# Optimization experiments

Measured on AMD Instinct MI355X. Metric: run time of the kernel, lower is better.

The kernel has to match this reference:

```python
import jax, jax.numpy as jnp
from jax import lax
import numpy as np

P = 24  # skip distance

def setup_inputs() -> dict:
    key = jax.random.key(0)
    k1, k2, k3 = jax.random.split(key, 3)
    B, T, F, U = 256, 192, 512, 512
    x = jax.random.normal(k1, (B, T, F), dtype=jnp.float32)
    # Glorot-ish scaled params (scale keeps relu candidate from exploding)
    kernel = jax.random.normal(k2, (F, 3 * U), dtype=jnp.float32) * (1.0 / np.sqrt(F))
    recurrent_kernel = jax.random.normal(k3, (U, 3 * U), dtype=jnp.float32) * (1.0 / np.sqrt(U))
    input_bias = jnp.zeros((3 * U,), dtype=jnp.float32)
    recurrent_bias = jnp.zeros((3 * U,), dtype=jnp.float32)
    return {"x": x, "kernel": kernel, "recurrent_kernel": recurrent_kernel,
            "input_bias": input_bias, "recurrent_bias": recurrent_bias}

def _gru_step(h, xc, kernel, recurrent_kernel, input_bias, recurrent_bias):
    # h, xc: [B, p, U] / [B, p, F] -- p independent skip-chains run as extra batch
    mx = xc @ kernel + input_bias            # [B, p, 3U]
    mi = h @ recurrent_kernel + recurrent_bias  # [B, p, 3U] (reset_after=True)
    xz, xr, xh = jnp.split(mx, 3, axis=-1)
    rz, rr, rh = jnp.split(mi, 3, axis=-1)
    z = jax.nn.sigmoid(xz + rz)
    r = jax.nn.sigmoid(xr + rr)
    hh = jax.nn.relu(xh + r * rh)            # activation='relu'
    return z * h + (1.0 - z) * hh

def reference(x, kernel, recurrent_kernel, input_bias, recurrent_bias):
    B, T, F = x.shape
    U = kernel.shape[1] // 3
    nc = T // P  # T chosen as multiple of p
    # chunk c, lane j  <->  timestep c*p + j; predecessor of (c, j) is (c-1, j) = t - p
    xs = x.reshape(B, nc, P, F).transpose(1, 0, 2, 3)  # [nc, B, p, F]
    h0 = jnp.zeros((B, P, U), dtype=x.dtype)

    def step(h, xc):
        hn = _gru_step(h, xc, kernel, recurrent_kernel, input_bias, recurrent_bias)
        return hn, hn

    _, ys = lax.scan(step, h0, xs)                      # [nc, B, p, U]
    outputs = ys.transpose(1, 0, 2, 3).reshape(B, T, U)  # [B, T, U]
    # return_sequences=False, return_state=False -> last timestep output
    return outputs[:, -1, :]
```

## Files before the change

### kernel.cpp

```cpp
#include <hip/hip_runtime.h>
#include <hip/hip_bf16.h>
#include <math.h>


typedef float f32x4 __attribute__((ext_vector_type(4)));
typedef short short8 __attribute__((ext_vector_type(8)));

#define BB 256
#define UU 512
#define KK 512
#define N3 1536

__device__ __forceinline__ float sigmoidf_(float s) {
    return 1.0f / (1.0f + __expf(-s));
}

__global__ __launch_bounds__(256)
void prologue(const float* __restrict__ ker, const float* __restrict__ rker,
              const float* __restrict__ x,
              __hip_bfloat16* __restrict__ Kt, __hip_bfloat16* __restrict__ Rtb,
              __hip_bfloat16* __restrict__ Xb)
{
    __shared__ float tile[32][33];
    const int blk = blockIdx.x;
    const int tid = threadIdx.x;
    if (blk < 1536) {
        const float* W = (blk < 768) ? ker : rker;
        __hip_bfloat16* Wt = (blk < 768) ? Kt : Rtb;
        const int b = (blk < 768) ? blk : blk - 768;
        const int xx = tid & 31, yy = tid >> 5;
        const int c0 = (b % 48) * 32;
        const int r0 = (b / 48) * 32;
        #pragma unroll
        for (int i = 0; i < 32; i += 8)
            tile[yy + i][xx] = W[(long)(r0 + yy + i) * N3 + c0 + xx];
        __syncthreads();
        #pragma unroll
        for (int i = 0; i < 32; i += 8)
            Wt[(long)(c0 + yy + i) * KK + r0 + xx] = __float2bfloat16(tile[xx][yy + i]);
    } else {
        const int idx = (blk - 1536) * 256 + tid;
        const int e = idx * 8;
        const int m = e >> 9;
        const int kk = e & 511;
        const int bb = m & 255, c = m >> 8;
        const float* src = x + (long)bb * (192 * 512) + (long)(c * 24 + 23) * 512 + kk;
        float4 v0 = *(const float4*)src;
        float4 v1 = *(const float4*)(src + 4);
        __hip_bfloat16* dst = Xb + (long)m * 512 + kk;
        dst[0] = __float2bfloat16(v0.x);
        dst[1] = __float2bfloat16(v0.y);
        dst[2] = __float2bfloat16(v0.z);
        dst[3] = __float2bfloat16(v0.w);
        dst[4] = __float2bfloat16(v1.x);
        dst[5] = __float2bfloat16(v1.y);
        dst[6] = __float2bfloat16(v1.z);
        dst[7] = __float2bfloat16(v1.w);
    }
}

__global__ __launch_bounds__(256)
void gemm_mx(const __hip_bfloat16* __restrict__ A,
             const __hip_bfloat16* __restrict__ Bt,
             const float* __restrict__ bias,
             float* __restrict__ C)
{
    __shared__ char Als[4096];
    __shared__ char Bls[8192];
    const int tid = threadIdx.x;
    const int lane = tid & 63;
    const int w = tid >> 6;
    const int wm = w >> 1, wn = w & 1;
    const int m0 = blockIdx.y * 64;
    const int n0 = blockIdx.x * 128;
    const int lr = lane & 15;
    const int hi = lane >> 4;

    const int srow = lane >> 2;
    const int scol = (lane & 3) * 16;

    const char* Ab = (const char*)A;
    const char* Bb = (const char*)Bt;

    f32x4 acc[2][4];
    #pragma unroll
    for (int i = 0; i < 2; ++i)
        #pragma unroll
        for (int j = 0; j < 4; ++j) acc[i][j] = {0.f, 0.f, 0.f, 0.f};

    for (int ks = 0; ks < 16; ++ks) {
        const long k0b = (long)ks * 64;
        __syncthreads();
        __builtin_amdgcn_global_load_lds(
            (const __attribute__((address_space(1))) unsigned int*)
                (Ab + (long)(m0 + w * 16 + srow) * 1024 + k0b + scol),
            (__attribute__((address_space(3))) unsigned int*)(Als + w * 1024),
            16, 0, 0);
        #pragma unroll
        for (int j = 0; j < 2; ++j)
            __builtin_amdgcn_global_load_lds(
                (const __attribute__((address_space(1))) unsigned int*)
                    (Bb + (long)(n0 + w * 32 + j * 16 + srow) * 1024 + k0b + scol),
                (__attribute__((address_space(3))) unsigned int*)
                    (Bls + (w * 2 + j) * 1024),
                16, 0, 0);
        __syncthreads();

        short8 a[2], b[4];
        #pragma unroll
        for (int i = 0; i < 2; ++i)
            a[i] = *(const short8*)(Als + (wm * 32 + i * 16 + lr) * 64 + hi * 16);
        #pragma unroll
        for (int j = 0; j < 4; ++j)
            b[j] = *(const short8*)(Bls + (wn * 64 + j * 16 + lr) * 64 + hi * 16);
        #pragma unroll
        for (int i = 0; i < 2; ++i)
            #pragma unroll
            for (int j = 0; j < 4; ++j)
                acc[i][j] = __builtin_amdgcn_mfma_f32_16x16x32_bf16(
                    a[i], b[j], acc[i][j], 0, 0, 0);
    }

    #pragma unroll
    for (int i = 0; i < 2; ++i)
        #pragma unroll
        for (int j = 0; j < 4; ++j) {
            const int u = n0 + wn * 64 + j * 16 + lr;
            const float bi = bias[u];
            #pragma unroll
            for (int q = 0; q < 4; ++q)
                C[(long)(m0 + wm * 32 + i * 16 + hi * 4 + q) * N3 + u]
                    = acc[i][j][q] + bi;
        }
}

__global__ __launch_bounds__(256)
void gru_step(const __hip_bfloat16* __restrict__ Rt,
              const float* __restrict__ rbias,
              const float* __restrict__ MXc,
              const char* __restrict__ hb_in,
              const float* __restrict__ hf_in,
              char* __restrict__ hb_out,
              float* __restrict__ hf_out,
              float* __restrict__ out,
              int last)
{
    __shared__ char Bls[96 * 1024];
    __shared__ char Als[32 * 1024];
    __shared__ char MXls[12288];
    const int tid = threadIdx.x;
    const int lane = tid & 63;
    const int w = tid >> 6;
    const int wy = w >> 1, wx = w & 1;
    const int by = blockIdx.x & 7;
    const int bx = blockIdx.x >> 3;
    const int lr = lane & 15;
    const int hi = lane >> 4;
    const int m0 = by * 32 + wy * 16;
    const int n0 = bx * 32;
    const int u  = n0 + wx * 16 + lr;

    {
        const char* RtB = (const char*)Rt;
        #pragma unroll
        for (int i = 0; i < 24; ++i) {
            const int j  = i * 4 + w;
            const int gt = j >> 5, cc = j & 31;
            const long srcoff = (long)(gt * 512 + n0 + cc) * 1024
                              + ((lane * 16) ^ ((j & 7) << 4));
            __builtin_amdgcn_global_load_lds(
                (const __attribute__((address_space(1))) unsigned int*)(RtB + srcoff),
                (__attribute__((address_space(3))) unsigned int*)(Bls + (long)j * 1024),
                16, 0, 0);
        }
    }
    #pragma unroll
    for (int i = 0; i < 8; ++i) {
        const int j = i * 4 + w;
        __builtin_amdgcn_global_load_lds(
            (const __attribute__((address_space(1))) unsigned int*)
                (hb_in + (long)(by * 32 + j) * 1024 + lane * 16),
            (__attribute__((address_space(3))) unsigned int*)(Als + (long)j * 1024),
            16, 0, 0);
    }
    {
        const char* MXb = (const char*)MXc;
        #pragma unroll
        for (int jj = 0; jj < 3; ++jj) {
            const int k = w + 4 * jj;
            const int gt = k >> 2, rblk = k & 3;
            const long src = (long)(by * 32 + rblk * 8 + (lane >> 3)) * 6144
                           + gt * 2048 + bx * 128 + (lane & 7) * 16;
            __builtin_amdgcn_global_load_lds(
                (const __attribute__((address_space(1))) unsigned int*)(MXb + src),
                (__attribute__((address_space(3))) unsigned int*)
                    (MXls + gt * 4096 + rblk * 1024),
                16, 0, 0);
        }
    }

    float hold[4];
    #pragma unroll
    for (int q = 0; q < 4; ++q)
        hold[q] = hf_in[(long)(m0 + hi * 4 + q) * UU + u];
    const float rbz = rbias[u];
    const float rbg = rbias[u + UU];
    const float rbh = rbias[u + 2 * UU];

    __syncthreads();

    f32x4 acc[3] = {{0.f,0.f,0.f,0.f},{0.f,0.f,0.f,0.f},{0.f,0.f,0.f,0.f}};
    #pragma unroll
    for (int kk = 0; kk < 16; ++kk) {
        const short8 a = *(const short8*)(Als + (wy * 16 + lr) * 1024
            + ((kk * 64 + hi * 16) ^ ((lr & 7) << 4)));
        #pragma unroll
        for (int gt = 0; gt < 3; ++gt) {
            const short8 b = *(const short8*)(Bls
                + (long)(gt * 32 + wx * 16 + lr) * 1024
                + ((kk * 64 + hi * 16) ^ ((lr & 7) << 4)));
            acc[gt] = __builtin_amdgcn_mfma_f32_16x16x32_bf16(a, b, acc[gt], 0, 0, 0);
        }
    }

    #pragma unroll
    for (int q = 0; q < 4; ++q) {
        const int rloc = wy * 16 + hi * 4 + q;
        const float xz = *(const float*)(MXls + 0 * 4096 + rloc * 128 + (wx * 16 + lr) * 4);
        const float xr = *(const float*)(MXls + 1 * 4096 + rloc * 128 + (wx * 16 + lr) * 4);
        const float xh = *(const float*)(MXls + 2 * 4096 + rloc * 128 + (wx * 16 + lr) * 4);
        const float z = sigmoidf_(xz + acc[0][q] + rbz);
        const float r = sigmoidf_(xr + acc[1][q] + rbg);
        const float cand = xh + r * (acc[2][q] + rbh);
        const float hh = fmaxf(cand, 0.0f);
        const float hn = z * hold[q] + (1.0f - z) * hh;
        const int m = m0 + hi * 4 + q;
        if (!last) {
            union { __hip_bfloat16 bf; unsigned short s; } cv;
            cv.bf = __float2bfloat16(hn);
            *(unsigned short*)(hb_out + (long)m * 1024
                + ((u * 2) ^ ((m & 7) << 4))) = cv.s;
            hf_out[(long)m * UU + u] = hn;
        } else {
            out[(long)m * UU + u] = hn;
        }
    }
}

__global__ __launch_bounds__(256)
void gru_step1(const __hip_bfloat16* __restrict__ Rt,
               const float* __restrict__ rbias,
               const float* __restrict__ MX1,
               const float* __restrict__ MX0,
               char* __restrict__ hb_out,
               float* __restrict__ hf_out)
{
    __shared__ char Bls[96 * 1024];
    __shared__ char Als[32 * 1024];
    __shared__ char MXls[12288];
    __shared__ float patchls[32 * 32];
    const int tid = threadIdx.x;
    const int lane = tid & 63;
    const int w = tid >> 6;
    const int wy = w >> 1, wx = w & 1;
    const int by = blockIdx.x & 7;
    const int bx = blockIdx.x >> 3;
    const int lr = lane & 15;
    const int hi = lane >> 4;
    const int m0 = by * 32 + wy * 16;
    const int n0 = bx * 32;
    const int u  = n0 + wx * 16 + lr;

    {
        const char* RtB = (const char*)Rt;
        #pragma unroll
        for (int i = 0; i < 24; ++i) {
            const int j  = i * 4 + w;
            const int gt = j >> 5, cc = j & 31;
            const long srcoff = (long)(gt * 512 + n0 + cc) * 1024
                              + ((lane * 16) ^ ((j & 7) << 4));
            __builtin_amdgcn_global_load_lds(
                (const __attribute__((address_space(1))) unsigned int*)(RtB + srcoff),
                (__attribute__((address_space(3))) unsigned int*)(Bls + (long)j * 1024),
                16, 0, 0);
        }
    }
    {
        const char* MXb = (const char*)MX1;
        #pragma unroll
        for (int jj = 0; jj < 3; ++jj) {
            const int k = w + 4 * jj;
            const int gt = k >> 2, rblk = k & 3;
            const long src = (long)(by * 32 + rblk * 8 + (lane >> 3)) * 6144
                           + gt * 2048 + bx * 128 + (lane & 7) * 16;
            __builtin_amdgcn_global_load_lds(
                (const __attribute__((address_space(1))) unsigned int*)(MXb + src),
                (__attribute__((address_space(3))) unsigned int*)
                    (MXls + gt * 4096 + rblk * 1024),
                16, 0, 0);
        }
    }
    const float rbz = rbias[u];
    const float rbg = rbias[u + UU];
    const float rbh = rbias[u + 2 * UU];

    {
        const int rt = tid >> 3;
        const int cb = (tid & 7) * 64;
        const float* mrow = MX0 + (long)(by * 32 + rt) * N3;
        #pragma unroll 4
        for (int j = 0; j < 64; j += 4) {
            const int col = cb + j;
            float4 xz = *(const float4*)(mrow + col);
            float4 xr = *(const float4*)(mrow + UU + col);
            float4 xh = *(const float4*)(mrow + 2 * UU + col);
            float4 bz = *(const float4*)(rbias + col);
            float4 br = *(const float4*)(rbias + UU + col);
            float4 bh = *(const float4*)(rbias + 2 * UU + col);
            float hv[4];
            hv[0] = (1.0f - sigmoidf_(xz.x + bz.x)) * fmaxf(xh.x + sigmoidf_(xr.x + br.x) * bh.x, 0.0f);
            hv[1] = (1.0f - sigmoidf_(xz.y + bz.y)) * fmaxf(xh.y + sigmoidf_(xr.y + br.y) * bh.y, 0.0f);
            hv[2] = (1.0f - sigmoidf_(xz.z + bz.z)) * fmaxf(xh.z + sigmoidf_(xr.z + br.z) * bh.z, 0.0f);
            hv[3] = (1.0f - sigmoidf_(xz.w + bz.w)) * fmaxf(xh.w + sigmoidf_(xr.w + br.w) * bh.w, 0.0f);
            #pragma unroll
            for (int e = 0; e < 4; ++e) {
                const int cc = col + e;
                union { __hip_bfloat16 bf; unsigned short s; } cv;
                cv.bf = __float2bfloat16(hv[e]);
                *(unsigned short*)(Als + rt * 1024 + ((cc * 2) ^ ((rt & 7) << 4))) = cv.s;
                if (cc >= n0 && cc < n0 + 32)
                    patchls[rt * 32 + (cc - n0)] = hv[e];
            }
        }
    }

    __syncthreads();

    f32x4 acc[3] = {{0.f,0.f,0.f,0.f},{0.f,0.f,0.f,0.f},{0.f,0.f,0.f,0.f}};
    #pragma unroll
    for (int kk = 0; kk < 16; ++kk) {
        const short8 a = *(const short8*)(Als + (wy * 16 + lr) * 1024
            + ((kk * 64 + hi * 16) ^ ((lr & 7) << 4)));
        #pragma unroll
        for (int gt = 0; gt < 3; ++gt) {
            const short8 b = *(const short8*)(Bls
                + (long)(gt * 32 + wx * 16 + lr) * 1024
                + ((kk * 64 + hi * 16) ^ ((lr & 7) << 4)));
            acc[gt] = __builtin_amdgcn_mfma_f32_16x16x32_bf16(a, b, acc[gt], 0, 0, 0);
        }
    }

    #pragma unroll
    for (int q = 0; q < 4; ++q) {
        const int rloc = wy * 16 + hi * 4 + q;
        const float xz = *(const float*)(MXls + 0 * 4096 + rloc * 128 + (wx * 16 + lr) * 4);
        const float xr = *(const float*)(MXls + 1 * 4096 + rloc * 128 + (wx * 16 + lr) * 4);
        const float xh = *(const float*)(MXls + 2 * 4096 + rloc * 128 + (wx * 16 + lr) * 4);
        const float hv = patchls[rloc * 32 + wx * 16 + lr];
        const float z = sigmoidf_(xz + acc[0][q] + rbz);
        const float r = sigmoidf_(xr + acc[1][q] + rbg);
        const float cand = xh + r * (acc[2][q] + rbh);
        const float hh = fmaxf(cand, 0.0f);
        const float hn = z * hv + (1.0f - z) * hh;
        const int m = m0 + hi * 4 + q;
        union { __hip_bfloat16 bf; unsigned short s; } cv;
        cv.bf = __float2bfloat16(hn);
        *(unsigned short*)(hb_out + (long)m * 1024
            + ((u * 2) ^ ((m & 7) << 4))) = cv.s;
        hf_out[(long)m * UU + u] = hn;
    }
}

extern "C" void kernel_launch(void* const* d_in, const int* in_sizes, int n_in,
                              void* d_out, int out_size, void* d_ws, size_t ws_size,
                              hipStream_t stream)
{
    const float* x     = (const float*)d_in[0];
    const float* ker   = (const float*)d_in[1];
    const float* rker  = (const float*)d_in[2];
    const float* ibias = (const float*)d_in[3];
    const float* rbias = (const float*)d_in[4];
    float* out = (float*)d_out;

    char* ws = (char*)d_ws;
    float*          MX   = (float*)ws;
    __hip_bfloat16* Xb   = (__hip_bfloat16*)(ws + 12582912);
    __hip_bfloat16* Kt   = (__hip_bfloat16*)(ws + 14680064);
    __hip_bfloat16* Rt   = (__hip_bfloat16*)(ws + 16252928);
    char*           hb0  = (char*)(ws + 17825792);
    char*           hb1  = (char*)(ws + 18087936);
    float*          hf0  = (float*)(ws + 12582912);
    float*          hf1  = (float*)(ws + 13107200);

    prologue<<<2048, 256, 0, stream>>>(ker, rker, x, Kt, Rt, Xb);

    gemm_mx<<<dim3(N3 / 128, 2048 / 64), 256, 0, stream>>>(Xb, Kt, ibias, MX);

    gru_step1<<<128, 256, 0, stream>>>(Rt, rbias, MX + (long)BB * N3, MX,
                                       hb0, hf0);

    for (int c = 2; c < 8; ++c) {
        const char*  hb_in = (c & 1) ? hb1 : hb0;
        const float* hf_in = (c & 1) ? hf1 : hf0;
        char*  hb_o = (c & 1) ? hb0 : hb1;
        float* hf_o = (c & 1) ? hf0 : hf1;
        gru_step<<<128, 256, 0, stream>>>(
            Rt, rbias, MX + (long)c * BB * N3, hb_in, hf_in,
            hb_o, hf_o, out, (c == 7) ? 1 : 0);
    }
}
```

Before: 66.97 us.

## Overlap input-projection GEMM tiles with recurrent GRU steps in shared launches

Splits the big input-projection GEMM so only the first two chunks are computed up front. The remaining chunks are computed by extra blocks appended to each recurrent step launch, one chunk ahead. Step 0 becomes a simple elementwise kernel, since h is zero, that also carries GEMM tiles, which removes the fused step-1 special case. The aim is to fill the idle CUs during the small 128-block recurrent steps and cut the serial GEMM time. In exchange, the GEMM blocks share the large LDS footprint of the step kernel, and the hf buffers move to a new workspace region.

```diff
diff --git a/kernel.cpp b/kernel.cpp
--- a/kernel.cpp
+++ b/kernel.cpp
@@ -59,23 +59,17 @@
     }
 }
 
-__global__ __launch_bounds__(256)
-void gemm_mx(const __hip_bfloat16* __restrict__ A,
-             const __hip_bfloat16* __restrict__ Bt,
-             const float* __restrict__ bias,
-             float* __restrict__ C)
-{
-    __shared__ char Als[4096];
-    __shared__ char Bls[8192];
+__device__ __forceinline__ void gemm_tile_dev(
+    const __hip_bfloat16* __restrict__ A, const __hip_bfloat16* __restrict__ Bt,
+    const float* __restrict__ bias, float* __restrict__ C,
+    int m0, int n0, char* Als, char* Bls)
+{
     const int tid = threadIdx.x;
     const int lane = tid & 63;
     const int w = tid >> 6;
     const int wm = w >> 1, wn = w & 1;
-    const int m0 = blockIdx.y * 64;
-    const int n0 = blockIdx.x * 128;
     const int lr = lane & 15;
     const int hi = lane >> 4;
-
     const int srow = lane >> 2;
     const int scol = (lane & 3) * 16;
 
@@ -132,6 +126,168 @@
                 C[(long)(m0 + wm * 32 + i * 16 + hi * 4 + q) * N3 + u]
                     = acc[i][j][q] + bi;
         }
+}
+
+__global__ __launch_bounds__(256)
+void gemm_mx(const __hip_bfloat16* __restrict__ A,
+             const __hip_bfloat16* __restrict__ Bt,
+             const float* __restrict__ bias,
+             float* __restrict__ C)
+{
+    __shared__ char Als[4096];
+    __shared__ char Bls[8192];
+    gemm_tile_dev(A, Bt, bias, C, blockIdx.y * 64, blockIdx.x * 128, Als, Bls);
+}
+
+__global__ __launch_bounds__(256)
+void gru_step0g(const float* __restrict__ MX0,
+                const float* __restrict__ rbias,
+                float* __restrict__ hf_out,
+                char* __restrict__ hb_out,
+                const __hip_bfloat16* __restrict__ Xb,
+                const __hip_bfloat16* __restrict__ Kt,
+                const float* __restrict__ ibias,
+                float* __restrict__ MX)
+{
+    __shared__ char GA[4096];
+    __shared__ char GB[8192];
+    if (blockIdx.x >= 512) {
+        const int g = blockIdx.x - 512;
+        const int gx = g % 12, gy = g / 12;
+        gemm_tile_dev(Xb, Kt, ibias, MX, 2 * 256 + gy * 64, gx * 128, GA, GB);
+        return;
+    }
+    const int idx = blockIdx.x * 256 + threadIdx.x;
+    const int b = idx >> 9;
+    const int u = idx & 511;
+    const float* mx = MX0 + (long)b * N3;
+    const float z = sigmoidf_(mx[u]          + rbias[u]);
+    const float r = sigmoidf_(mx[u + UU]     + rbias[u + UU]);
+    const float cand = mx[u + 2 * UU] + r * rbias[u + 2 * UU];
+    const float hh = fmaxf(cand, 0.0f);
+    const float hn = (1.0f - z) * hh;
+    hf_out[idx] = hn;
+    union { __hip_bfloat16 bf; unsigned short s; } cv;
+    cv.bf = __float2bfloat16(hn);
+    *(unsigned short*)(hb_out + (long)b * 1024 + ((u * 2) ^ ((b & 7) << 4))) = cv.s;
+}
+
+__global__ __launch_bounds__(256)
+void gru_stepg(const __hip_bfloat16* __restrict__ Rt,
+               const float* __restrict__ rbias,
+               const float* __restrict__ MXc,
+               const char* __restrict__ hb_in,
+               const float* __restrict__ hf_in,
+               char* __restrict__ hb_out,
+               float* __restrict__ hf_out,
+               const __hip_bfloat16* __restrict__ Xb,
+               const __hip_bfloat16* __restrict__ Kt,
+               const float* __restrict__ ibias,
+               float* __restrict__ MX,
+               int cg)
+{
+    __shared__ char Bls[96 * 1024];
+    __shared__ char Als[32 * 1024];
+    __shared__ char MXls[12288];
+    if (blockIdx.x >= 128) {
+        const int g = blockIdx.x - 128;
+        const int gx = g % 12, gy = g / 12;
+        gemm_tile_dev(Xb, Kt, ibias, MX, cg * 256 + gy * 64, gx * 128, Als, Bls);
+        return;
+    }
+    const int tid = threadIdx.x;
+    const int lane = tid & 63;
+    const int w = tid >> 6;
+    const int wy = w >> 1, wx = w & 1;
+    const int by = blockIdx.x & 7;
+    const int bx = blockIdx.x >> 3;
+    const int lr = lane & 15;
+    const int hi = lane >> 4;
+    const int m0 = by * 32 + wy * 16;
+    const int n0 = bx * 32;
+    const int u  = n0 + wx * 16 + lr;
+
+    {
+        const char* RtB = (const char*)Rt;
+        #pragma unroll
+        for (int i = 0; i < 24; ++i) {
+            const int j  = i * 4 + w;
+            const int gt = j >> 5, cc = j & 31;
+            const long srcoff = (long)(gt * 512 + n0 + cc) * 1024
+                              + ((lane * 16) ^ ((j & 7) << 4));
+            __builtin_amdgcn_global_load_lds(
+                (const __attribute__((address_space(1))) unsigned int*)(RtB + srcoff),
+                (__attribute__((address_space(3))) unsigned int*)(Bls + (long)j * 1024),
+                16, 0, 0);
+        }
+    }
+    #pragma unroll
+    for (int i = 0; i < 8; ++i) {
+        const int j = i * 4 + w;
+        __builtin_amdgcn_global_load_lds(
+            (const __attribute__((address_space(1))) unsigned int*)
+                (hb_in + (long)(by * 32 + j) * 1024 + lane * 16),
+            (__attribute__((address_space(3))) unsigned int*)(Als + (long)j * 1024),
+            16, 0, 0);
+    }
+    {
+        const char* MXb = (const char*)MXc;
+        #pragma unroll
+        for (int jj = 0; jj < 3; ++jj) {
+            const int k = w + 4 * jj;
+            const int gt = k >> 2, rblk = k & 3;
+            const long src = (long)(by * 32 + rblk * 8 + (lane >> 3)) * 6144
+                           + gt * 2048 + bx * 128 + (lane & 7) * 16;
+            __builtin_amdgcn_global_load_lds(
+                (const __attribute__((address_space(1))) unsigned int*)(MXb + src),
+                (__attribute__((address_space(3))) unsigned int*)
+                    (MXls + gt * 4096 + rblk * 1024),
+                16, 0, 0);
+        }
+    }
+
+    float hold[4];
+    #pragma unroll
+    for (int q = 0; q < 4; ++q)
+        hold[q] = hf_in[(long)(m0 + hi * 4 + q) * UU + u];
+    const float rbz = rbias[u];
+    const float rbg = rbias[u + UU];
+    const float rbh = rbias[u + 2 * UU];
+
+    __syncthreads();
+
+    f32x4 acc[3] = {{0.f,0.f,0.f,0.f},{0.f,0.f,0.f,0.f},{0.f,0.f,0.f,0.f}};
+    #pragma unroll
+    for (int kk = 0; kk < 16; ++kk) {
+        const short8 a = *(const short8*)(Als + (wy * 16 + lr) * 1024
+            + ((kk * 64 + hi * 16) ^ ((lr & 7) << 4)));
+        #pragma unroll
+        for (int gt = 0; gt < 3; ++gt) {
+            const short8 b = *(const short8*)(Bls
+                + (long)(gt * 32 + wx * 16 + lr) * 1024
+                + ((kk * 64 + hi * 16) ^ ((lr & 7) << 4)));
+            acc[gt] = __builtin_amdgcn_mfma_f32_16x16x32_bf16(a, b, acc[gt], 0, 0, 0);
+        }
+    }
+
+    #pragma unroll
+    for (int q = 0; q < 4; ++q) {
+        const int rloc = wy * 16 + hi * 4 + q;
+        const float xz = *(const float*)(MXls + 0 * 4096 + rloc * 128 + (wx * 16 + lr) * 4);
+        const float xr = *(const float*)(MXls + 1 * 4096 + rloc * 128 + (wx * 16 + lr) * 4);
+        const float xh = *(const float*)(MXls + 2 * 4096 + rloc * 128 + (wx * 16 + lr) * 4);
+        const float z = sigmoidf_(xz + acc[0][q] + rbz);
+        const float r = sigmoidf_(xr + acc[1][q] + rbg);
+        const float cand = xh + r * (acc[2][q] + rbh);
+        const float hh = fmaxf(cand, 0.0f);
+        const float hn = z * hold[q] + (1.0f - z) * hh;
+        const int m = m0 + hi * 4 + q;
+        union { __hip_bfloat16 bf; unsigned short s; } cv;
+        cv.bf = __float2bfloat16(hn);
+        *(unsigned short*)(hb_out + (long)m * 1024
+            + ((u * 2) ^ ((m & 7) << 4))) = cv.s;
+        hf_out[(long)m * UU + u] = hn;
+    }
 }
 
 __global__ __launch_bounds__(256)
@@ -247,130 +403,6 @@
     }
 }
 
-__global__ __launch_bounds__(256)
-void gru_step1(const __hip_bfloat16* __restrict__ Rt,
-               const float* __restrict__ rbias,
-               const float* __restrict__ MX1,
-               const float* __restrict__ MX0,
-               char* __restrict__ hb_out,
-               float* __restrict__ hf_out)
-{
-    __shared__ char Bls[96 * 1024];
-    __shared__ char Als[32 * 1024];
-    __shared__ char MXls[12288];
-    __shared__ float patchls[32 * 32];
-    const int tid = threadIdx.x;
-    const int lane = tid & 63;
-    const int w = tid >> 6;
-    const int wy = w >> 1, wx = w & 1;
-    const int by = blockIdx.x & 7;
-    const int bx = blockIdx.x >> 3;
-    const int lr = lane & 15;
-    const int hi = lane >> 4;
-    const int m0 = by * 32 + wy * 16;
-    const int n0 = bx * 32;
-    const int u  = n0 + wx * 16 + lr;
-
-    {
-        const char* RtB = (const char*)Rt;
-        #pragma unroll
-        for (int i = 0; i < 24; ++i) {
-            const int j  = i * 4 + w;
-            const int gt = j >> 5, cc = j & 31;
-            const long srcoff = (long)(gt * 512 + n0 + cc) * 1024
-                              + ((lane * 16) ^ ((j & 7) << 4));
-            __builtin_amdgcn_global_load_lds(
-                (const __attribute__((address_space(1))) unsigned int*)(RtB + srcoff),
-                (__attribute__((address_space(3))) unsigned int*)(Bls + (long)j * 1024),
-                16, 0, 0);
-        }
-    }
-    {
-        const char* MXb = (const char*)MX1;
-        #pragma unroll
-        for (int jj = 0; jj < 3; ++jj) {
-            const int k = w + 4 * jj;
-            const int gt = k >> 2, rblk = k & 3;
-            const long src = (long)(by * 32 + rblk * 8 + (lane >> 3)) * 6144
-                           + gt * 2048 + bx * 128 + (lane & 7) * 16;
-            __builtin_amdgcn_global_load_lds(
-                (const __attribute__((address_space(1))) unsigned int*)(MXb + src),
-                (__attribute__((address_space(3))) unsigned int*)
-                    (MXls + gt * 4096 + rblk * 1024),
-                16, 0, 0);
-        }
-    }
-    const float rbz = rbias[u];
-    const float rbg = rbias[u + UU];
-    const float rbh = rbias[u + 2 * UU];
-
-    {
-        const int rt = tid >> 3;
-        const int cb = (tid & 7) * 64;
-        const float* mrow = MX0 + (long)(by * 32 + rt) * N3;
-        #pragma unroll 4
-        for (int j = 0; j < 64; j += 4) {
-            const int col = cb + j;
-            float4 xz = *(const float4*)(mrow + col);
-            float4 xr = *(const float4*)(mrow + UU + col);
-            float4 xh = *(const float4*)(mrow + 2 * UU + col);
-            float4 bz = *(const float4*)(rbias + col);
-            float4 br = *(const float4*)(rbias + UU + col);
-            float4 bh = *(const float4*)(rbias + 2 * UU + col);
-            float hv[4];
-            hv[0] = (1.0f - sigmoidf_(xz.x + bz.x)) * fmaxf(xh.x + sigmoidf_(xr.x + br.x) * bh.x, 0.0f);
-            hv[1] = (1.0f - sigmoidf_(xz.y + bz.y)) * fmaxf(xh.y + sigmoidf_(xr.y + br.y) * bh.y, 0.0f);
-            hv[2] = (1.0f - sigmoidf_(xz.z + bz.z)) * fmaxf(xh.z + sigmoidf_(xr.z + br.z) * bh.z, 0.0f);
-            hv[3] = (1.0f - sigmoidf_(xz.w + bz.w)) * fmaxf(xh.w + sigmoidf_(xr.w + br.w) * bh.w, 0.0f);
-            #pragma unroll
-            for (int e = 0; e < 4; ++e) {
-                const int cc = col + e;
-                union { __hip_bfloat16 bf; unsigned short s; } cv;
-                cv.bf = __float2bfloat16(hv[e]);
-                *(unsigned short*)(Als + rt * 1024 + ((cc * 2) ^ ((rt & 7) << 4))) = cv.s;
-                if (cc >= n0 && cc < n0 + 32)
-                    patchls[rt * 32 + (cc - n0)] = hv[e];
-            }
-        }
-    }
-
-    __syncthreads();
-
-    f32x4 acc[3] = {{0.f,0.f,0.f,0.f},{0.f,0.f,0.f,0.f},{0.f,0.f,0.f,0.f}};
-    #pragma unroll
-    for (int kk = 0; kk < 16; ++kk) {
-        const short8 a = *(const short8*)(Als + (wy * 16 + lr) * 1024
-            + ((kk * 64 + hi * 16) ^ ((lr & 7) << 4)));
-        #pragma unroll
-        for (int gt = 0; gt < 3; ++gt) {
-            const short8 b = *(const short8*)(Bls
-                + (long)(gt * 32 + wx * 16 + lr) * 1024
-                + ((kk * 64 + hi * 16) ^ ((lr & 7) << 4)));
-            acc[gt] = __builtin_amdgcn_mfma_f32_16x16x32_bf16(a, b, acc[gt], 0, 0, 0);
-        }
-    }
-
-    #pragma unroll
-    for (int q = 0; q < 4; ++q) {
-        const int rloc = wy * 16 + hi * 4 + q;
-        const float xz = *(const float*)(MXls + 0 * 4096 + rloc * 128 + (wx * 16 + lr) * 4);
-        const float xr = *(const float*)(MXls + 1 * 4096 + rloc * 128 + (wx * 16 + lr) * 4);
-        const float xh = *(const float*)(MXls + 2 * 4096 + rloc * 128 + (wx * 16 + lr) * 4);
-        const float hv = patchls[rloc * 32 + wx * 16 + lr];
-        const float z = sigmoidf_(xz + acc[0][q] + rbz);
-        const float r = sigmoidf_(xr + acc[1][q] + rbg);
-        const float cand = xh + r * (acc[2][q] + rbh);
-        const float hh = fmaxf(cand, 0.0f);
-        const float hn = z * hv + (1.0f - z) * hh;
-        const int m = m0 + hi * 4 + q;
-        union { __hip_bfloat16 bf; unsigned short s; } cv;
-        cv.bf = __float2bfloat16(hn);
-        *(unsigned short*)(hb_out + (long)m * 1024
-            + ((u * 2) ^ ((m & 7) << 4))) = cv.s;
-        hf_out[(long)m * UU + u] = hn;
-    }
-}
-
 extern "C" void kernel_launch(void* const* d_in, const int* in_sizes, int n_in,
                               void* d_out, int out_size, void* d_ws, size_t ws_size,
                               hipStream_t stream)
@@ -389,17 +421,27 @@
     __hip_bfloat16* Rt   = (__hip_bfloat16*)(ws + 16252928);
     char*           hb0  = (char*)(ws + 17825792);
     char*           hb1  = (char*)(ws + 18087936);
-    float*          hf0  = (float*)(ws + 12582912);
-    float*          hf1  = (float*)(ws + 13107200);
+    float*          hf0  = (float*)(ws + 18350080);
+    float*          hf1  = (float*)(ws + 18874368);
 
     prologue<<<2048, 256, 0, stream>>>(ker, rker, x, Kt, Rt, Xb);
 
-    gemm_mx<<<dim3(N3 / 128, 2048 / 64), 256, 0, stream>>>(Xb, Kt, ibias, MX);
-
-    gru_step1<<<128, 256, 0, stream>>>(Rt, rbias, MX + (long)BB * N3, MX,
-                                       hb0, hf0);
-
-    for (int c = 2; c < 8; ++c) {
+    gemm_mx<<<dim3(N3 / 128, 8), 256, 0, stream>>>(Xb, Kt, ibias, MX);
+
+    gru_step0g<<<560, 256, 0, stream>>>(MX, rbias, hf1, hb1,
+                                        Xb, Kt, ibias, MX);
+
+    for (int c = 1; c <= 5; ++c) {
+        const char*  hb_in = (c & 1) ? hb1 : hb0;
+        const float* hf_in = (c & 1) ? hf1 : hf0;
+        char*  hb_o = (c & 1) ? hb0 : hb1;
+        float* hf_o = (c & 1) ? hf0 : hf1;
+        gru_stepg<<<176, 256, 0, stream>>>(
+            Rt, rbias, MX + (long)c * BB * N3, hb_in, hf_in,
+            hb_o, hf_o, Xb, Kt, ibias, MX, c + 2);
+    }
+
+    for (int c = 6; c < 8; ++c) {
         const char*  hb_in = (c & 1) ? hb1 : hb0;
         const float* hf_in = (c & 1) ? hf1 : hf0;
         char*  hb_o = (c & 1) ? hb0 : hb1;
```

After: 82.27 us. +22.8%, slower.
